# Kernel tuning notes

Hardware: AMD Instinct MI355X
Metric: run time of the kernel (lower is better)

Reference implementation:

```python
import jax, jax.numpy as jnp
import numpy as np

NPOINT, NSAMPLE, RADIUS = 1024, 32, 0.2
BN_EPS = 1e-5


def _fps(xyz, npoint):
    # Farthest point sampling. Torch version starts from a random index; we use
    # index 0 deterministically (same algorithm, fixed seed point).
    B, N, _ = xyz.shape

    def step(carry, _):
        distance, farthest = carry                               # [B,N], [B]
        centroid = jnp.take_along_axis(xyz, farthest[:, None, None], axis=1)  # [B,1,3]
        d = jnp.sum((xyz - centroid) ** 2, axis=-1)              # [B,N]
        distance = jnp.minimum(distance, d)
        nxt = jnp.argmax(distance, axis=-1).astype(jnp.int32)
        return (distance, nxt), farthest

    init = (jnp.full((B, N), 1e10, xyz.dtype), jnp.zeros((B,), jnp.int32))
    _, cents = jax.lax.scan(step, init, None, length=npoint)     # [npoint,B]
    return jnp.transpose(cents)                                  # [B,npoint]


def _ball_query(radius, nsample, xyz, new_xyz):
    # Sort-based ball query, exactly as the torch reference (pad with first idx).
    B, N, _ = xyz.shape
    sq = -2.0 * jnp.einsum('bsc,bnc->bsn', new_xyz, xyz)
    sq = sq + jnp.sum(new_xyz ** 2, -1)[:, :, None] + jnp.sum(xyz ** 2, -1)[:, None, :]
    idx = jnp.where(sq > radius * radius, N, jnp.arange(N, dtype=jnp.int32))  # [B,S,N]
    idx = jnp.sort(idx, axis=-1)[:, :, :nsample]                 # [B,S,nsample]
    first = idx[:, :, :1]
    return jnp.where(idx == N, first, idx)


def setup_inputs() -> dict:
    key = jax.random.key(0)
    ks = jax.random.split(key, 4)
    B, N = 8, 8192
    d = {"x": jax.random.uniform(ks[0], (B, N, 3), jnp.float32)}
    mlp = [3, 64, 64, 128]
    for i in range(3):
        cin, cout = mlp[i], mlp[i + 1]
        d[f"W{i+1}"] = jax.random.normal(ks[i + 1], (cout, cin), jnp.float32) * 0.1
        d[f"b{i+1}"] = jnp.zeros((cout,), jnp.float32)
        d[f"g{i+1}"] = jnp.ones((cout,), jnp.float32)
        d[f"be{i+1}"] = jnp.zeros((cout,), jnp.float32)
    return d


def reference(x, W1, b1, g1, be1, W2, b2, g2, be2, W3, b3, g3, be3):
    # sample_and_group (points=None)
    cents = _fps(x, NPOINT)                                      # [B,npoint]
    new_x = jnp.take_along_axis(x, cents[:, :, None], axis=1)    # [B,npoint,3]
    idx = _ball_query(RADIUS, NSAMPLE, x, new_x)                 # [B,npoint,nsample]
    grouped = jax.vmap(lambda p, i: p[i])(x, idx)                # [B,npoint,nsample,3]
    h = jnp.transpose(grouped - new_x[:, :, None, :], (0, 3, 2, 1))  # [B,3,nsample,npoint]

    # grouped 1x1 conv + BatchNorm (training-mode batch stats) + ReLU
    for W, b, g, be in ((W1, b1, g1, be1), (W2, b2, g2, be2), (W3, b3, g3, be3)):
        y = jnp.einsum('bcns,oc->bons', h, W) + b[None, :, None, None]
        mean = jnp.mean(y, axis=(0, 2, 3), keepdims=True)
        var = jnp.mean((y - mean) ** 2, axis=(0, 2, 3), keepdims=True)
        h = jax.nn.relu(g[None, :, None, None] * (y - mean) * jax.lax.rsqrt(var + BN_EPS)
                        + be[None, :, None, None])

    out = jnp.transpose(jnp.max(h, axis=2), (0, 2, 1))           # [B,npoint,128]
    return new_x, out
```

## Files before the change

### kernel.cpp

```cpp
#include <hip/hip_runtime.h>
#include <stdint.h>

constexpr int NB = 8;
constexpr int NN = 8192;
constexpr int NS = 1024;
constexpr int NK = 32;
constexpr int PTOT = NB * NS * NK;

#define R2C 0.039999999105930328f

__device__ unsigned short g_cents[NB * NS];
__device__ unsigned short g_idx[NB * NS * NK];
__device__ float g_stat1[12];
__device__ float g_stat2[4160];
__device__ float g_stat3[4160];
__device__ float g_st1[128];
__device__ float g_st2[128];
__device__ float g_st3[256];
__device__ float g_h2[(size_t)PTOT * 64];

__global__ __launch_bounds__(256, 4) void k_zero(){
  const int tid = threadIdx.x;
  for (int i = tid; i < 4160; i += 256){ g_stat2[i] = 0.f; g_stat3[i] = 0.f; }
  if (tid < 12) g_stat1[tid] = 0.f;
}

template<int C, int R>
__device__ __forceinline__ void rstep64(uint32_t& kh, uint32_t& kl){
  uint32_t oh = (uint32_t)__builtin_amdgcn_update_dpp(0, (int)kh, C, R, 0xf, false);
  uint32_t ol = (uint32_t)__builtin_amdgcn_update_dpp(0, (int)kl, C, R, 0xf, false);
  uint64_t o = ((uint64_t)oh << 32) | ol;
  uint64_t k = ((uint64_t)kh << 32) | kl;
  if (o > k){ kh = oh; kl = ol; }
}

__global__ __launch_bounds__(512)
__attribute__((amdgpu_waves_per_eu(2, 2)))
void k_fps(const float* __restrict__ x){
  __shared__ float lp[NN * 3];
  __shared__ uint2 part[16];
  const int b = blockIdx.x;
  const int t = threadIdx.x;
  const int lane = t & 63;
  const int w = t >> 6;
  const float* xb = x + b * NN * 3;
  float px[16], py[16], pz[16], dd[16];
#pragma unroll
  for (int j = 0; j < 16; j++){
    int p = t + 512 * j;
    px[j] = xb[p*3+0]; py[j] = xb[p*3+1]; pz[j] = xb[p*3+2];
    dd[j] = 1e10f;
  }
#pragma unroll
  for (int j = 0; j < 16; j++){
    asm volatile("" : "+v"(px[j]), "+v"(py[j]), "+v"(pz[j]));
  }
  for (int i = t; i < NN*3; i += 512) lp[i] = xb[i];
  float cx = xb[0], cy = xb[1], cz = xb[2];
  if (t == 0) g_cents[b*NS] = 0;
  __syncthreads();
  for (int s = 0; s < NS-1; s++){
    float bv = -1.0f; int bi = 0x7fffffff;
#pragma unroll
    for (int j = 0; j < 16; j++){
      float dx = __fsub_rn(px[j], cx);
      float dy = __fsub_rn(py[j], cy);
      float dz = __fsub_rn(pz[j], cz);
      float d  = __fadd_rn(__fadd_rn(__fmul_rn(dx,dx), __fmul_rn(dy,dy)), __fmul_rn(dz,dz));
      float nd = fminf(dd[j], d);
      dd[j] = nd;
      if (nd > bv){ bv = nd; bi = t + 512*j; }
    }
    uint32_t kh = __float_as_uint(bv);
    uint32_t kl = ~(uint32_t)bi;
    rstep64<0x111, 0xf>(kh, kl);
    rstep64<0x112, 0xf>(kh, kl);
    rstep64<0x114, 0xf>(kh, kl);
    rstep64<0x118, 0xf>(kh, kl);
    rstep64<0x142, 0xa>(kh, kl);
    rstep64<0x143, 0xc>(kh, kl);
    const int pb = (s & 1) << 3;
    if (lane == 63) part[pb + w] = make_uint2(kl, kh);
    asm volatile("s_waitcnt lgkmcnt(0)\n\ts_barrier" ::: "memory");
    uint2 pr = part[pb + (lane & 7)];
    uint32_t qh = pr.y, ql = pr.x;
    rstep64<0x111, 0xf>(qh, ql);
    rstep64<0x112, 0xf>(qh, ql);
    rstep64<0x114, 0xf>(qh, ql);
    int widx = ~__builtin_amdgcn_readlane((int)ql, 7);
    const float* cp = lp + widx*3;
    cx = cp[0]; cy = cp[1]; cz = cp[2];
    if (t == 0) g_cents[b*NS + s + 1] = (unsigned short)widx;
  }
}

__device__ __forceinline__ void ballq_wave(const float* __restrict__ xb,
                                           int c, unsigned short* og,
                                           float* __restrict__ oc){
  const int lane = threadIdx.x & 63;
  const float ax = xb[c*3+0], ay = xb[c*3+1], az = xb[c*3+2];
  if (lane == 0){ oc[0] = ax; oc[1] = ay; oc[2] = az; }
  const float na = __fadd_rn(__fadd_rn(__fmul_rn(ax,ax), __fmul_rn(ay,ay)), __fmul_rn(az,az));
  int cnt = 0, first = -1;
  for (int base = 0; base < NN && cnt < NK; base += 64){
    int n = base + lane;
    float bx = xb[n*3+0], by = xb[n*3+1], bz = xb[n*3+2];
    float dot = __fadd_rn(__fadd_rn(__fmul_rn(ax,bx), __fmul_rn(ay,by)), __fmul_rn(az,bz));
    float nb  = __fadd_rn(__fadd_rn(__fmul_rn(bx,bx), __fmul_rn(by,by)), __fmul_rn(bz,bz));
    float sq  = __fadd_rn(__fadd_rn(__fmul_rn(-2.0f, dot), na), nb);
    bool valid = !(sq > R2C);
    unsigned long long m = __ballot(valid);
    if (first < 0 && m) first = base + (int)__builtin_ctzll(m);
    int pre = __popcll(m & ((1ull << lane) - 1ull));
    int pos = cnt + pre;
    if (valid && pos < NK) og[pos] = (unsigned short)n;
    cnt += __popcll(m);
  }
  if (cnt < NK && lane >= cnt && lane < NK) og[lane] = (unsigned short)first;
}

__global__ __launch_bounds__(256, 4) void k_ballq(const float* __restrict__ x,
                                                  float* __restrict__ out){
  const int g = blockIdx.x * 4 + (threadIdx.x >> 6);
  const float* xb = x + (g >> 10) * NN * 3;
  ballq_wave(xb, (int)g_cents[g], g_idx + (size_t)g * NK, out + (size_t)g * 3);
}

__global__ __launch_bounds__(256, 4) void k_stat1(const float* __restrict__ x){
  __shared__ unsigned int idxs_u[512];
  __shared__ float gc[32][3];
  unsigned short* idxs = (unsigned short*)idxs_u;
  const int tid = threadIdx.x;
  const int g0 = blockIdx.x * 32;
  const float* xb = x + (g0 >> 10) * NN * 3;
  for (int i = tid; i < 512; i += 256)
    idxs_u[i] = ((const unsigned int*)(g_idx + (size_t)g0 * NK))[i];
  if (tid < 32){
    int cc = g_cents[g0 + tid];
    gc[tid][0]=xb[cc*3+0]; gc[tid][1]=xb[cc*3+1]; gc[tid][2]=xb[cc*3+2];
  }
  __syncthreads();
  float a[12];
#pragma unroll
  for (int i = 0; i < 12; i++) a[i] = 0.f;
  for (int u = 0; u < 4; u++){
    int sid = u*256 + tid;
    int lg = sid >> 5, kk = sid & 31;
    int ii = idxs[lg*32 + kk];
    float hx = xb[ii*3+0] - gc[lg][0];
    float hy = xb[ii*3+1] - gc[lg][1];
    float hz = xb[ii*3+2] - gc[lg][2];
    a[0]+=hx; a[1]+=hy; a[2]+=hz;
    a[3]+=hx*hx; a[4]+=hx*hy; a[5]+=hx*hz;
    a[6]+=hy*hx; a[7]+=hy*hy; a[8]+=hy*hz;
    a[9]+=hz*hx; a[10]+=hz*hy; a[11]+=hz*hz;
  }
#pragma unroll
  for (int i = 0; i < 12; i++){
#pragma unroll
    for (int off = 32; off > 0; off >>= 1) a[i] += __shfl_down(a[i], off);
  }
  if ((tid & 63) == 0){
#pragma unroll
    for (int i = 0; i < 12; i++) atomicAdd(&g_stat1[i], a[i]);
  }
}

__global__ __launch_bounds__(256, 4) void k_fold(const float* __restrict__ W,
                       const float* __restrict__ gg,
                       const float* __restrict__ be,
                       int which, int Cin, int Cout){
  const float* stats = (which == 0) ? g_stat1 : (which == 1) ? g_stat2 : g_stat3;
  float* st = (which == 0) ? g_st1 : (which == 1) ? g_st2 : g_st3;
  __shared__ float mu[64];
  __shared__ float partl[256];
  __shared__ float s_l[64*65];
  __shared__ float w_l[128*65];
  const int tid = threadIdx.x;
  const float invP = 1.0f / (float)PTOT;
  for (int i = tid; i < Cout*Cin; i += 256) w_l[(i/Cin)*65 + (i%Cin)] = W[i];
  for (int i = tid; i < Cin*Cin; i += 256) s_l[(i/Cin)*65 + (i%Cin)] = stats[Cin + i] * invP;
  if (tid < Cin) mu[tid] = stats[tid] * invP;
  __syncthreads();
  const int nparts = 256 / Cout;
  const int c = tid % Cout;
  const int prt = tid / Cout;
  float q = 0.f;
  for (int i = prt; i < Cin; i += nparts){
    float wi = w_l[c*65 + i];
    float r = 0.f;
    for (int j = 0; j < Cin; j++)
      r += s_l[i*65 + j] * w_l[c*65 + j];
    q += wi * r;
  }
  partl[tid] = q;
  __syncthreads();
  if (prt == 0){
    for (int p2 = 1; p2 < nparts; p2++) q += partl[p2*Cout + c];
    float ml = 0.f;
    for (int j = 0; j < Cin; j++) ml += w_l[c*65 + j] * mu[j];
    float var = q - ml*ml;
    float inv = 1.0f / sqrtf(var + 1e-5f);
    float sc = gg[c] * inv;
    float tc = be[c] - sc * ml;
    st[c] = sc; st[Cout + c] = tc;
  }
}

__global__ __launch_bounds__(256, 2) void k_stat2(const float* __restrict__ x,
                                                  const float* __restrict__ W1){
  __shared__ unsigned int idxs_u[512];
  __shared__ float gc[32][3];
  __shared__ float w1t[3][64];
  __shared__ float s1v[64], t1v[64];
  __shared__ float tile[128*68];
  __shared__ float muacc[64];
  unsigned short* idxs = (unsigned short*)idxs_u;
  const int tid = threadIdx.x;
  const int g0 = blockIdx.x * 32;
  const float* xb = x + (g0 >> 10) * NN * 3;
  for (int i = tid; i < 512; i += 256)
    idxs_u[i] = ((const unsigned int*)(g_idx + (size_t)g0 * NK))[i];
  if (tid < 32){
    int cc = g_cents[g0 + tid];
    gc[tid][0]=xb[cc*3+0]; gc[tid][1]=xb[cc*3+1]; gc[tid][2]=xb[cc*3+2];
  }
  if (tid < 64){
    w1t[0][tid]=W1[tid*3+0]; w1t[1][tid]=W1[tid*3+1]; w1t[2][tid]=W1[tid*3+2];
    s1v[tid]=g_st1[tid]; t1v[tid]=g_st1[64+tid];
    muacc[tid]=0.f;
  }
  float acc[4][4];
#pragma unroll
  for (int r=0;r<4;r++)
#pragma unroll
    for (int q=0;q<4;q++) acc[r][q]=0.f;
  const int ti = tid & 15, tj = tid >> 4;
  const int pl = tid & 127;
  const int ch0 = (tid >> 7) * 32;
  __syncthreads();
  for (int u = 0; u < 8; u++){
    int sid = u*128 + pl;
    int lg = sid >> 5, kk = sid & 31;
    int ii = idxs[lg*32 + kk];
    float hx = xb[ii*3+0] - gc[lg][0];
    float hy = xb[ii*3+1] - gc[lg][1];
    float hz = xb[ii*3+2] - gc[lg][2];
    float* row = &tile[pl*68 + ch0];
    float* h2g = &g_h2[((size_t)g0*32 + sid)*64 + ch0];
#pragma unroll
    for (int cq = 0; cq < 8; cq++){
      int c = ch0 + cq*4;
      float y0 = fmaf(w1t[0][c+0],hx, fmaf(w1t[1][c+0],hy, w1t[2][c+0]*hz));
      float y1 = fmaf(w1t[0][c+1],hx, fmaf(w1t[1][c+1],hy, w1t[2][c+1]*hz));
      float y2 = fmaf(w1t[0][c+2],hx, fmaf(w1t[1][c+2],hy, w1t[2][c+2]*hz));
      float y3 = fmaf(w1t[0][c+3],hx, fmaf(w1t[1][c+3],hy, w1t[2][c+3]*hz));
      float4 hv;
      hv.x = fmaxf(fmaf(s1v[c+0],y0,t1v[c+0]), 0.f);
      hv.y = fmaxf(fmaf(s1v[c+1],y1,t1v[c+1]), 0.f);
      hv.z = fmaxf(fmaf(s1v[c+2],y2,t1v[c+2]), 0.f);
      hv.w = fmaxf(fmaf(s1v[c+3],y3,t1v[c+3]), 0.f);
      *(float4*)&row[cq*4] = hv;
      *(float4*)&h2g[cq*4] = hv;
    }
    __syncthreads();
    const float4* t4 = (const float4*)tile;
#pragma unroll 4
    for (int p = 0; p < 128; p++){
      float4 av = t4[p*17 + ti];
      float4 bv = t4[p*17 + tj];
      acc[0][0]=fmaf(av.x,bv.x,acc[0][0]); acc[0][1]=fmaf(av.x,bv.y,acc[0][1]);
      acc[0][2]=fmaf(av.x,bv.z,acc[0][2]); acc[0][3]=fmaf(av.x,bv.w,acc[0][3]);
      acc[1][0]=fmaf(av.y,bv.x,acc[1][0]); acc[1][1]=fmaf(av.y,bv.y,acc[1][1]);
      acc[1][2]=fmaf(av.y,bv.z,acc[1][2]); acc[1][3]=fmaf(av.y,bv.w,acc[1][3]);
      acc[2][0]=fmaf(av.z,bv.x,acc[2][0]); acc[2][1]=fmaf(av.z,bv.y,acc[2][1]);
      acc[2][2]=fmaf(av.z,bv.z,acc[2][2]); acc[2][3]=fmaf(av.z,bv.w,acc[2][3]);
      acc[3][0]=fmaf(av.w,bv.x,acc[3][0]); acc[3][1]=fmaf(av.w,bv.y,acc[3][1]);
      acc[3][2]=fmaf(av.w,bv.z,acc[3][2]); acc[3][3]=fmaf(av.w,bv.w,acc[3][3]);
    }
    if (tid < 64){
      float m = 0.f;
      for (int p = 0; p < 128; p++) m += tile[p*68 + tid];
      muacc[tid] += m;
    }
    __syncthreads();
  }
  if (tid < 64) atomicAdd(&g_stat2[tid], muacc[tid]);
#pragma unroll
  for (int r=0;r<4;r++)
#pragma unroll
    for (int q=0;q<4;q++)
      atomicAdd(&g_stat2[64 + (ti*4+r)*64 + (tj*4+q)], acc[r][q]);
}

__global__ __launch_bounds__(256, 2) void k_stat3(const float* __restrict__ x,
                                                  const float* __restrict__ W1,
                                                  const float* __restrict__ W2){
  __shared__ float s2v[64], t2v[64];
  __shared__ float w2f[4096];
  __shared__ float tile[128*68];
  __shared__ float muacc[64];
  const int tid = threadIdx.x;
  const int g0 = blockIdx.x * 32;
  if (tid < 64){
    s2v[tid]=g_st2[tid]; t2v[tid]=g_st2[64+tid];
    muacc[tid]=0.f;
  }
#pragma unroll
  for (int e = 0; e < 16; e++) w2f[tid + e*256] = W2[tid + e*256];
  float acc[4][4];
#pragma unroll
  for (int r=0;r<4;r++)
#pragma unroll
    for (int q=0;q<4;q++) acc[r][q]=0.f;
  const int ti = tid & 15, tj = tid >> 4;
  const int pl = tid & 127;
  const int ch0 = (tid >> 7) * 32;
  __syncthreads();
  for (int u = 0; u < 8; u++){
    int sid = u*128 + pl;
    float h2r[64];
    const float4* h2p = (const float4*)&g_h2[((size_t)g0*32 + sid)*64];
#pragma unroll
    for (int j4 = 0; j4 < 16; j4++){
      float4 v = h2p[j4];
      h2r[j4*4+0]=v.x; h2r[j4*4+1]=v.y; h2r[j4*4+2]=v.z; h2r[j4*4+3]=v.w;
    }
    float* row = &tile[pl*68];
    for (int c = ch0; c < ch0 + 32; c++){
      const float4* wr = (const float4*)&w2f[c*64];
      float y = 0.f;
#pragma unroll
      for (int j4 = 0; j4 < 16; j4++){
        float4 wv = wr[j4];
        y = fmaf(wv.x, h2r[j4*4+0], y);
        y = fmaf(wv.y, h2r[j4*4+1], y);
        y = fmaf(wv.z, h2r[j4*4+2], y);
        y = fmaf(wv.w, h2r[j4*4+3], y);
      }
      row[c] = fmaxf(fmaf(s2v[c], y, t2v[c]), 0.f);
    }
    __syncthreads();
    const float4* t4 = (const float4*)tile;
#pragma unroll 4
    for (int p = 0; p < 128; p++){
      float4 av = t4[p*17 + ti];
      float4 bv = t4[p*17 + tj];
      acc[0][0]=fmaf(av.x,bv.x,acc[0][0]); acc[0][1]=fmaf(av.x,bv.y,acc[0][1]);
      acc[0][2]=fmaf(av.x,bv.z,acc[0][2]); acc[0][3]=fmaf(av.x,bv.w,acc[0][3]);
      acc[1][0]=fmaf(av.y,bv.x,acc[1][0]); acc[1][1]=fmaf(av.y,bv.y,acc[1][1]);
      acc[1][2]=fmaf(av.y,bv.z,acc[1][2]); acc[1][3]=fmaf(av.y,bv.w,acc[1][3]);
      acc[2][0]=fmaf(av.z,bv.x,acc[2][0]); acc[2][1]=fmaf(av.z,bv.y,acc[2][1]);
      acc[2][2]=fmaf(av.z,bv.z,acc[2][2]); acc[2][3]=fmaf(av.z,bv.w,acc[2][3]);
      acc[3][0]=fmaf(av.w,bv.x,acc[3][0]); acc[3][1]=fmaf(av.w,bv.y,acc[3][1]);
      acc[3][2]=fmaf(av.w,bv.z,acc[3][2]); acc[3][3]=fmaf(av.w,bv.w,acc[3][3]);
    }
    if (tid < 64){
      float m = 0.f;
      for (int p = 0; p < 128; p++) m += tile[p*68 + tid];
      muacc[tid] += m;
    }
    __syncthreads();
  }
  if (tid < 64) atomicAdd(&g_stat3[tid], muacc[tid]);
#pragma unroll
  for (int r=0;r<4;r++)
#pragma unroll
    for (int q=0;q<4;q++)
      atomicAdd(&g_stat3[64 + (ti*4+r)*64 + (tj*4+q)], acc[r][q]);
}

__global__ __launch_bounds__(256, 2) void k_final(const float* __restrict__ x,
    const float* __restrict__ W1,
    const float* __restrict__ W2,
    const float* __restrict__ W3,
    float* __restrict__ out){
  __shared__ float s2v[64], t2v[64], s3v[128], t3v[128];
  __shared__ float h2t[32*68];
  __shared__ float h3t[32*68];
  __shared__ float mx[2][128];
  const int tid = threadIdx.x;
  const int g0 = blockIdx.x * 4;
  if (tid < 64){
    s2v[tid]=g_st2[tid]; t2v[tid]=g_st2[64+tid];
  }
  if (tid < 128){ s3v[tid]=g_st3[tid]; t3v[tid]=g_st3[128+tid]; }
  __syncthreads();
  for (int gi = 0; gi < 4; gi++){
    {
      const float* src = &g_h2[(size_t)(g0 + gi) * 32 * 64];
#pragma unroll
      for (int u = 0; u < 8; u++){
        int v = tid + u * 256;
        int kk = v >> 6, c = v & 63;
        h2t[kk*68 + c] = src[v];
      }
    }
    __syncthreads();
    {
      const int c2 = tid & 63, kq = tid >> 6;
      float wv2[64];
      const float4* wrow = (const float4*)(W2 + c2*64);
#pragma unroll
      for (int q = 0; q < 16; q++){
        float4 uv = wrow[q];
        wv2[q*4+0]=uv.x; wv2[q*4+1]=uv.y; wv2[q*4+2]=uv.z; wv2[q*4+3]=uv.w;
      }
#pragma unroll
      for (int k2 = 0; k2 < 8; k2++){
        int kk = kq*8 + k2;
        const float4* hr = (const float4*)&h2t[kk*68];
        float y = 0.f;
#pragma unroll
        for (int j4 = 0; j4 < 16; j4++){
          float4 hv = hr[j4];
          y = fmaf(wv2[j4*4+0], hv.x, y);
          y = fmaf(wv2[j4*4+1], hv.y, y);
          y = fmaf(wv2[j4*4+2], hv.z, y);
          y = fmaf(wv2[j4*4+3], hv.w, y);
        }
        h3t[kk*68 + c2] = fmaxf(fmaf(s2v[c2], y, t2v[c2]), 0.f);
      }
    }
    __syncthreads();
    {
      const int c3 = tid & 127, half = tid >> 7;
      float wv3[64];
      const float4* wrow = (const float4*)(W3 + c3*64);
#pragma unroll
      for (int q = 0; q < 16; q++){
        float4 uv = wrow[q];
        wv3[q*4+0]=uv.x; wv3[q*4+1]=uv.y; wv3[q*4+2]=uv.z; wv3[q*4+3]=uv.w;
      }
      float m = -1e30f;
#pragma unroll
      for (int k2 = 0; k2 < 16; k2++){
        int kk = half*16 + k2;
        const float4* hr = (const float4*)&h3t[kk*68];
        float y = 0.f;
#pragma unroll
        for (int j4 = 0; j4 < 16; j4++){
          float4 hv = hr[j4];
          y = fmaf(wv3[j4*4+0], hv.x, y);
          y = fmaf(wv3[j4*4+1], hv.y, y);
          y = fmaf(wv3[j4*4+2], hv.z, y);
          y = fmaf(wv3[j4*4+3], hv.w, y);
        }
        float h4 = fmaxf(fmaf(s3v[c3], y, t3v[c3]), 0.f);
        m = fmaxf(m, h4);
      }
      mx[half][c3] = m;
    }
    __syncthreads();
    if (tid < 128){
      float m = fmaxf(mx[0][tid], mx[1][tid]);
      out[24576 + ((g0 + gi) << 7) + tid] = m;
    }
    __syncthreads();
  }
}

extern "C" void kernel_launch(void* const* d_in, const int* in_sizes, int n_in,
                              void* d_out, int out_size, void* d_ws, size_t ws_size,
                              hipStream_t stream){
  const float* x   = (const float*)d_in[0];
  const float* W1  = (const float*)d_in[1];
  const float* g1  = (const float*)d_in[3];
  const float* be1 = (const float*)d_in[4];
  const float* W2  = (const float*)d_in[5];
  const float* g2  = (const float*)d_in[7];
  const float* be2 = (const float*)d_in[8];
  const float* W3  = (const float*)d_in[9];
  const float* g3  = (const float*)d_in[11];
  const float* be3 = (const float*)d_in[12];
  float* out = (float*)d_out;
  (void)d_ws; (void)ws_size; (void)in_sizes; (void)n_in; (void)out_size;

  k_zero<<<1, 256, 0, stream>>>();
  k_fps<<<NB, 512, 0, stream>>>(x);
  k_ballq<<<(NB*NS)/4, 256, 0, stream>>>(x, out);
  k_stat1<<<256, 256, 0, stream>>>(x);
  k_fold<<<1, 256, 0, stream>>>(W1, g1, be1, 0, 3, 64);
  k_stat2<<<256, 256, 0, stream>>>(x, W1);
  k_fold<<<1, 256, 0, stream>>>(W2, g2, be2, 1, 64, 64);
  k_stat3<<<256, 256, 0, stream>>>(x, W1, W2);
  k_fold<<<1, 256, 0, stream>>>(W3, g3, be3, 2, 64, 128);
  k_final<<<2048, 256, 0, stream>>>(x, W1, W2, W3, out);
}
```

Before: 1.710 ms.

## Fold BN-stat folding into consumer kernels and drop zero/fold launches

Removes the separate zeroing kernel by clearing the stat buffers in block 0 of the ball-query kernel. The BN1 and BN2 scale/shift folding now runs redundantly inside every block of the stat2 and stat3 kernels, which removes two single-block launches. The BN3 fold becomes an 8-block kernel. The aim is to cut launch count and serialized single-block work, at the price of redundant per-block compute: the 64x64x64 quadratic form is recomputed in each of the 256 stat3 blocks.

```diff
diff --git a/kernel.cpp b/kernel.cpp
--- a/kernel.cpp
+++ b/kernel.cpp
@@ -14,16 +14,9 @@
 __device__ float g_stat1[12];
 __device__ float g_stat2[4160];
 __device__ float g_stat3[4160];
-__device__ float g_st1[128];
 __device__ float g_st2[128];
 __device__ float g_st3[256];
 __device__ float g_h2[(size_t)PTOT * 64];
-
-__global__ __launch_bounds__(256, 4) void k_zero(){
-  const int tid = threadIdx.x;
-  for (int i = tid; i < 4160; i += 256){ g_stat2[i] = 0.f; g_stat3[i] = 0.f; }
-  if (tid < 12) g_stat1[tid] = 0.f;
-}
 
 template<int C, int R>
 __device__ __forceinline__ void rstep64(uint32_t& kh, uint32_t& kl){
@@ -121,6 +114,11 @@
 
 __global__ __launch_bounds__(256, 4) void k_ballq(const float* __restrict__ x,
                                                   float* __restrict__ out){
+  if (blockIdx.x == 0){
+    const int tid = threadIdx.x;
+    for (int i = tid; i < 4160; i += 256){ g_stat2[i] = 0.f; g_stat3[i] = 0.f; }
+    if (tid < 12) g_stat1[tid] = 0.f;
+  }
   const int g = blockIdx.x * 4 + (threadIdx.x >> 6);
   const float* xb = x + (g >> 10) * NN * 3;
   ballq_wave(xb, (int)g_cents[g], g_idx + (size_t)g * NK, out + (size_t)g * 3);
@@ -166,59 +164,24 @@
   }
 }
 
-__global__ __launch_bounds__(256, 4) void k_fold(const float* __restrict__ W,
-                       const float* __restrict__ gg,
-                       const float* __restrict__ be,
-                       int which, int Cin, int Cout){
-  const float* stats = (which == 0) ? g_stat1 : (which == 1) ? g_stat2 : g_stat3;
-  float* st = (which == 0) ? g_st1 : (which == 1) ? g_st2 : g_st3;
-  __shared__ float mu[64];
-  __shared__ float partl[256];
-  __shared__ float s_l[64*65];
-  __shared__ float w_l[128*65];
-  const int tid = threadIdx.x;
-  const float invP = 1.0f / (float)PTOT;
-  for (int i = tid; i < Cout*Cin; i += 256) w_l[(i/Cin)*65 + (i%Cin)] = W[i];
-  for (int i = tid; i < Cin*Cin; i += 256) s_l[(i/Cin)*65 + (i%Cin)] = stats[Cin + i] * invP;
-  if (tid < Cin) mu[tid] = stats[tid] * invP;
-  __syncthreads();
-  const int nparts = 256 / Cout;
-  const int c = tid % Cout;
-  const int prt = tid / Cout;
-  float q = 0.f;
-  for (int i = prt; i < Cin; i += nparts){
-    float wi = w_l[c*65 + i];
-    float r = 0.f;
-    for (int j = 0; j < Cin; j++)
-      r += s_l[i*65 + j] * w_l[c*65 + j];
-    q += wi * r;
-  }
-  partl[tid] = q;
-  __syncthreads();
-  if (prt == 0){
-    for (int p2 = 1; p2 < nparts; p2++) q += partl[p2*Cout + c];
-    float ml = 0.f;
-    for (int j = 0; j < Cin; j++) ml += w_l[c*65 + j] * mu[j];
-    float var = q - ml*ml;
-    float inv = 1.0f / sqrtf(var + 1e-5f);
-    float sc = gg[c] * inv;
-    float tc = be[c] - sc * ml;
-    st[c] = sc; st[Cout + c] = tc;
-  }
-}
-
 __global__ __launch_bounds__(256, 2) void k_stat2(const float* __restrict__ x,
-                                                  const float* __restrict__ W1){
+                                                  const float* __restrict__ W1,
+                                                  const float* __restrict__ g1,
+                                                  const float* __restrict__ be1){
   __shared__ unsigned int idxs_u[512];
   __shared__ float gc[32][3];
   __shared__ float w1t[3][64];
   __shared__ float s1v[64], t1v[64];
   __shared__ float tile[128*68];
   __shared__ float muacc[64];
+  __shared__ float ss[9];
+  __shared__ float mu1[3];
+  __shared__ float partl[256];
   unsigned short* idxs = (unsigned short*)idxs_u;
   const int tid = threadIdx.x;
   const int g0 = blockIdx.x * 32;
   const float* xb = x + (g0 >> 10) * NN * 3;
+  const float invP = 1.0f / (float)PTOT;
   for (int i = tid; i < 512; i += 256)
     idxs_u[i] = ((const unsigned int*)(g_idx + (size_t)g0 * NK))[i];
   if (tid < 32){
@@ -227,8 +190,31 @@
   }
   if (tid < 64){
     w1t[0][tid]=W1[tid*3+0]; w1t[1][tid]=W1[tid*3+1]; w1t[2][tid]=W1[tid*3+2];
-    s1v[tid]=g_st1[tid]; t1v[tid]=g_st1[64+tid];
     muacc[tid]=0.f;
+  }
+  if (tid < 9) ss[tid] = g_stat1[3 + tid] * invP;
+  if (tid < 3) mu1[tid] = g_stat1[tid] * invP;
+  __syncthreads();
+  {
+    const int c = tid % 64, prt = tid / 64;
+    float q = 0.f;
+    for (int i = prt; i < 3; i += 4){
+      float wi = w1t[i][c];
+      float r = 0.f;
+      for (int j = 0; j < 3; j++) r += ss[i*3 + j] * w1t[j][c];
+      q += wi * r;
+    }
+    partl[tid] = q;
+    __syncthreads();
+    if (prt == 0){
+      for (int p2 = 1; p2 < 4; p2++) q += partl[p2*64 + c];
+      float ml = 0.f;
+      for (int j = 0; j < 3; j++) ml += w1t[j][c] * mu1[j];
+      float var = q - ml*ml;
+      float inv = 1.0f / sqrtf(var + 1e-5f);
+      float sc = g1[c] * inv;
+      s1v[c] = sc; t1v[c] = be1[c] - sc * ml;
+    }
   }
   float acc[4][4];
 #pragma unroll
@@ -293,21 +279,51 @@
       atomicAdd(&g_stat2[64 + (ti*4+r)*64 + (tj*4+q)], acc[r][q]);
 }
 
-__global__ __launch_bounds__(256, 2) void k_stat3(const float* __restrict__ x,
-                                                  const float* __restrict__ W1,
-                                                  const float* __restrict__ W2){
+__global__ __launch_bounds__(256, 2) void k_stat3(const float* __restrict__ W2,
+                                                  const float* __restrict__ g2,
+                                                  const float* __restrict__ be2){
   __shared__ float s2v[64], t2v[64];
   __shared__ float w2f[4096];
   __shared__ float tile[128*68];
   __shared__ float muacc[64];
+  __shared__ float mu2[64];
+  __shared__ float partl[256];
   const int tid = threadIdx.x;
   const int g0 = blockIdx.x * 32;
-  if (tid < 64){
-    s2v[tid]=g_st2[tid]; t2v[tid]=g_st2[64+tid];
-    muacc[tid]=0.f;
-  }
-#pragma unroll
-  for (int e = 0; e < 16; e++) w2f[tid + e*256] = W2[tid + e*256];
+  const float invP = 1.0f / (float)PTOT;
+  {
+    float* s_l = tile;
+    float* w_l = tile + 64*65;
+    for (int i = tid; i < 4096; i += 256) w_l[(i>>6)*65 + (i&63)] = W2[i];
+    for (int i = tid; i < 4096; i += 256) s_l[(i>>6)*65 + (i&63)] = g_stat2[64 + i] * invP;
+    if (tid < 64){ mu2[tid] = g_stat2[tid] * invP; muacc[tid] = 0.f; }
+#pragma unroll
+    for (int e = 0; e < 16; e++) w2f[tid + e*256] = W2[tid + e*256];
+    __syncthreads();
+    const int c = tid % 64, prt = tid / 64;
+    float q = 0.f;
+    for (int i = prt; i < 64; i += 4){
+      float wi = w_l[c*65 + i];
+      float r = 0.f;
+      for (int j = 0; j < 64; j++)
+        r += s_l[i*65 + j] * w_l[c*65 + j];
+      q += wi * r;
+    }
+    partl[tid] = q;
+    __syncthreads();
+    if (prt == 0){
+      for (int p2 = 1; p2 < 4; p2++) q += partl[p2*64 + c];
+      float ml = 0.f;
+      for (int j = 0; j < 64; j++) ml += w_l[c*65 + j] * mu2[j];
+      float var = q - ml*ml;
+      float inv = 1.0f / sqrtf(var + 1e-5f);
+      float sc = g2[c] * inv;
+      float tc = be2[c] - sc * ml;
+      s2v[c] = sc; t2v[c] = tc;
+      if (blockIdx.x == 0){ g_st2[c] = sc; g_st2[64 + c] = tc; }
+    }
+    __syncthreads();
+  }
   float acc[4][4];
 #pragma unroll
   for (int r=0;r<4;r++)
@@ -316,7 +332,6 @@
   const int ti = tid & 15, tj = tid >> 4;
   const int pl = tid & 127;
   const int ch0 = (tid >> 7) * 32;
-  __syncthreads();
   for (int u = 0; u < 8; u++){
     int sid = u*128 + pl;
     float h2r[64];
@@ -370,9 +385,48 @@
       atomicAdd(&g_stat3[64 + (ti*4+r)*64 + (tj*4+q)], acc[r][q]);
 }
 
-__global__ __launch_bounds__(256, 2) void k_final(const float* __restrict__ x,
-    const float* __restrict__ W1,
-    const float* __restrict__ W2,
+__global__ __launch_bounds__(256, 4) void k_fold3(const float* __restrict__ W3,
+                                                  const float* __restrict__ g3,
+                                                  const float* __restrict__ be3){
+  __shared__ float s_l[64*65];
+  __shared__ float w_l[16*65];
+  __shared__ float mu[64];
+  __shared__ float partl[32];
+  const int tid = threadIdx.x;
+  const int cb = blockIdx.x * 16;
+  const float invP = 1.0f / (float)PTOT;
+  for (int i = tid; i < 4096; i += 256) s_l[(i>>6)*65 + (i&63)] = g_stat3[64 + i] * invP;
+  for (int i = tid; i < 16*64; i += 256) w_l[(i>>6)*65 + (i&63)] = W3[(cb + (i>>6))*64 + (i&63)];
+  if (tid < 64) mu[tid] = g_stat3[tid] * invP;
+  __syncthreads();
+  if (tid < 32){
+    const int cl = tid & 15, prt = tid >> 4;
+    float q = 0.f;
+    for (int i = prt; i < 64; i += 2){
+      float wi = w_l[cl*65 + i];
+      float r = 0.f;
+      for (int j = 0; j < 64; j++)
+        r += s_l[i*65 + j] * w_l[cl*65 + j];
+      q += wi * r;
+    }
+    partl[tid] = q;
+  }
+  __syncthreads();
+  if (tid < 16){
+    const int cl = tid;
+    const int c = cb + cl;
+    float q = partl[cl] + partl[16 + cl];
+    float ml = 0.f;
+    for (int j = 0; j < 64; j++) ml += w_l[cl*65 + j] * mu[j];
+    float var = q - ml*ml;
+    float inv = 1.0f / sqrtf(var + 1e-5f);
+    float sc = g3[c] * inv;
+    float tc = be3[c] - sc * ml;
+    g_st3[c] = sc; g_st3[128 + c] = tc;
+  }
+}
+
+__global__ __launch_bounds__(256, 2) void k_final(const float* __restrict__ W2,
     const float* __restrict__ W3,
     float* __restrict__ out){
   __shared__ float s2v[64], t2v[64], s3v[128], t3v[128];
@@ -476,14 +530,11 @@
   float* out = (float*)d_out;
   (void)d_ws; (void)ws_size; (void)in_sizes; (void)n_in; (void)out_size;
 
-  k_zero<<<1, 256, 0, stream>>>();
   k_fps<<<NB, 512, 0, stream>>>(x);
   k_ballq<<<(NB*NS)/4, 256, 0, stream>>>(x, out);
   k_stat1<<<256, 256, 0, stream>>>(x);
-  k_fold<<<1, 256, 0, stream>>>(W1, g1, be1, 0, 3, 64);
-  k_stat2<<<256, 256, 0, stream>>>(x, W1);
-  k_fold<<<1, 256, 0, stream>>>(W2, g2, be2, 1, 64, 64);
-  k_stat3<<<256, 256, 0, stream>>>(x, W1, W2);
-  k_fold<<<1, 256, 0, stream>>>(W3, g3, be3, 2, 64, 128);
-  k_final<<<2048, 256, 0, stream>>>(x, W1, W2, W3, out);
-}
+  k_stat2<<<256, 256, 0, stream>>>(x, W1, g1, be1);
+  k_stat3<<<256, 256, 0, stream>>>(W2, g2, be2);
+  k_fold3<<<8, 256, 0, stream>>>(W3, g3, be3);
+  k_final<<<2048, 256, 0, stream>>>(W2, W3, out);
+}
```

Result: no change. 1.686 ms, median of 2 (-1.4%).
